# Kernel tuning notes

Measured on AMD Instinct MI355X. Metric: run time of the kernel, lower is better.

The kernel has to match this reference:

```python
import jax, jax.numpy as jnp
import numpy as np

EPS = 1e-5  # matches repo calc_mean_std eps


def _mvn(x):
    # mean-variance normalization per (B, C) over spatial dims, unbiased var (torch default)
    B, C, H, W = x.shape
    xf = x.reshape(B, C, H * W)
    m = xf.mean(-1, keepdims=True)
    v = xf.var(-1, ddof=1, keepdims=True)
    return ((xf - m) / jnp.sqrt(v + EPS)).reshape(x.shape)


def _conv1x1(x, w, b):
    # 1x1 conv == per-pixel channel mixing
    return jnp.einsum('oc,bchw->bohw', w, x) + b[None, :, None, None]


def _content_sa(x, Wp, bp):
    B, C, H, W = x.shape
    n = H * W
    xn = _mvn(x)
    q = _conv1x1(xn, Wp[0], bp[0]).reshape(B, C, n)  # f
    k = _conv1x1(xn, Wp[1], bp[1]).reshape(B, C, n)  # g
    energy = jnp.einsum('bci,bcj->bij', q, k)        # [B, N, N]
    attn = jax.nn.softmax(energy, axis=-1)
    v = _conv1x1(x, Wp[2], bp[2]).reshape(B, C, n)   # h
    out = jnp.einsum('bcj,bij->bci', v, attn).reshape(B, C, H, W)
    return _conv1x1(out, Wp[3], bp[3]) + x


def _style_sa(x, Wp, bp):
    B, C, H, W = x.shape
    n = H * W
    f = _conv1x1(x, Wp[0], bp[0]).reshape(B, C, n)
    g = _conv1x1(x, Wp[1], bp[1]).reshape(B, C, n)
    energy = jnp.einsum('bci,bdi->bcd', f, g)        # [B, C, C] channel attention
    attn = jax.nn.softmax(energy, axis=-1)
    h = _conv1x1(_mvn(x), Wp[2], bp[2]).reshape(B, C, n)
    out = jnp.einsum('bdc,bdi->bci', attn, h).reshape(B, C, H, W)  # attn^T @ h
    return _conv1x1(out, Wp[3], bp[3]) + x


def _ca(c, s, Wp, bp):
    B, C, Hc, Wc = c.shape
    nc = Hc * Wc
    _, _, Hs, Ws = s.shape
    ns = Hs * Ws
    q = _conv1x1(_mvn(c), Wp[0], bp[0]).reshape(B, C, nc)
    k = _conv1x1(_mvn(s), Wp[1], bp[1]).reshape(B, C, ns)
    energy = jnp.einsum('bci,bcj->bij', q, k)        # [B, Nc, Ns]
    attn = jax.nn.softmax(energy, axis=-1)
    v = _conv1x1(s, Wp[2], bp[2]).reshape(B, C, ns)
    out = jnp.einsum('bcj,bij->bci', v, attn).reshape(B, C, Hc, Wc)
    return _conv1x1(out, Wp[3], bp[3]) + c


def setup_inputs() -> dict:
    key = jax.random.key(0)
    ks = jax.random.split(key, 8)
    B, C, H, W = 4, 512, 64, 64
    scale = 0.02
    return {
        'content_feat': jax.random.normal(ks[0], (B, C, H, W), jnp.float32),
        'style_feat': jax.random.normal(ks[1], (B, C, H, W), jnp.float32),
        'csa_w': jax.random.normal(ks[2], (4, C, C), jnp.float32) * scale,
        'csa_b': jnp.zeros((4, C), jnp.float32),
        'ssa_w': jax.random.normal(ks[3], (4, C, C), jnp.float32) * scale,
        'ssa_b': jnp.zeros((4, C), jnp.float32),
        'ca_w': jax.random.normal(ks[4], (4, C, C), jnp.float32) * scale,
        'ca_b': jnp.zeros((4, C), jnp.float32),
    }


def reference(content_feat, style_feat, csa_w, csa_b, ssa_w, ssa_b, ca_w, ca_b):
    cf = _content_sa(content_feat, csa_w, csa_b)
    sf = _style_sa(style_feat, ssa_w, ssa_b)
    return _ca(cf, sf, ca_w, ca_b)
```

## Files before the change

kernel.cpp:

```cpp
#include <hip/hip_runtime.h>
#include <math.h>


#define B_ 4
#define C_ 512
#define N_ 4096
#define TM 128
#define TN 128

typedef unsigned short u16;
typedef __attribute__((ext_vector_type(8))) short s8v;
typedef __attribute__((ext_vector_type(4))) float f4v;

__device__ __forceinline__ u16 f2bf(float x) {
  unsigned u = __float_as_uint(x);
  return (u16)((u + 0x7fffu + ((u >> 16) & 1u)) >> 16);
}

__device__ __forceinline__ void gload16(const void* g, void* l) {
  __builtin_amdgcn_global_load_lds(
      (const __attribute__((address_space(1))) unsigned int*)g,
      (__attribute__((address_space(3))) unsigned int*)l, 16, 0, 0);
}

__device__ __forceinline__ float wave_red_sum(float v) {
#pragma unroll
  for (int off = 32; off > 0; off >>= 1) v += __shfl_xor(v, off, 64);
  return v;
}
__device__ __forceinline__ float wave_red_max(float v) {
#pragma unroll
  for (int off = 32; off > 0; off >>= 1) v = fmaxf(v, __shfl_xor(v, off, 64));
  return v;
}

__global__ __launch_bounds__(256) void row_stats_k(const float* __restrict__ x,
                                                   float* __restrict__ mean,
                                                   float* __restrict__ rstd) {
  long row = blockIdx.x;
  const float* p = x + row * (long)N_;
  int t = threadIdx.x;
  float s = 0.f, ss = 0.f;
  for (int i = t * 4; i < N_; i += 1024) {
    float4 v = *(const float4*)(p + i);
    s += v.x + v.y + v.z + v.w;
    ss += v.x * v.x + v.y * v.y + v.z * v.z + v.w * v.w;
  }
  __shared__ float rs_[4], rss_[4];
  int wid = t >> 6, lane = t & 63;
  s = wave_red_sum(s);
  ss = wave_red_sum(ss);
  if (lane == 0) { rs_[wid] = s; rss_[wid] = ss; }
  __syncthreads();
  if (t == 0) {
    float S = rs_[0] + rs_[1] + rs_[2] + rs_[3];
    float SS = rss_[0] + rss_[1] + rss_[2] + rss_[3];
    float m = S / (float)N_;
    float var = (SS - (float)N_ * m * m) / (float)(N_ - 1);
    mean[row] = m;
    rstd[row] = rsqrtf(var + 1e-5f);
  }
}

__global__ __launch_bounds__(256) void cvt_arr_k(const float* __restrict__ in,
                                                 u16* __restrict__ o, long n) {
  long i = ((long)blockIdx.x * 256 + threadIdx.x) * 4;
  if (i >= n) return;
  float4 v = *(const float4*)(in + i);
  *(ushort4*)(o + i) =
      make_ushort4(f2bf(v.x), f2bf(v.y), f2bf(v.z), f2bf(v.w));
}

template <bool HAS2>
__global__ __launch_bounds__(256) void t_cvt_k(
    const float* __restrict__ X, const float* __restrict__ mean,
    const float* __restrict__ rstd, u16* __restrict__ o1,
    u16* __restrict__ o2) {
  __shared__ float tile[64][68];
  const int b = blockIdx.z;
  const int c0 = blockIdx.y * 64, i0 = blockIdx.x * 64;
  const int t = threadIdx.x;
  const int tr = t >> 4, tc = (t & 15) << 2;
  const long CN = (long)C_ * N_;
  const float* Xb = X + (long)b * CN;
#pragma unroll
  for (int p2 = 0; p2 < 4; ++p2) {
    int c = p2 * 16 + tr;
    float4 v = *(const float4*)(Xb + (long)(c0 + c) * N_ + i0 + tc);
    tile[c][tc] = v.x;
    tile[c][tc + 1] = v.y;
    tile[c][tc + 2] = v.z;
    tile[c][tc + 3] = v.w;
  }
  __syncthreads();
  float mv[4], rv[4];
#pragma unroll
  for (int j = 0; j < 4; ++j) {
    mv[j] = mean[b * C_ + c0 + tc + j];
    rv[j] = rstd[b * C_ + c0 + tc + j];
  }
#pragma unroll
  for (int p2 = 0; p2 < 4; ++p2) {
    int ir = p2 * 16 + tr;
    long off = (long)b * CN + (long)(i0 + ir) * C_ + c0 + tc;
    u16 h1[4], h2[4];
#pragma unroll
    for (int j = 0; j < 4; ++j) {
      float v = tile[tc + j][ir];
      if (HAS2) h2[j] = f2bf(v);
      h1[j] = f2bf((v - mv[j]) * rv[j]);
    }
    *(ushort4*)(o1 + off) = make_ushort4(h1[0], h1[1], h1[2], h1[3]);
    if (HAS2) *(ushort4*)(o2 + off) = make_ushort4(h2[0], h2[1], h2[2], h2[3]);
  }
}

__global__ __launch_bounds__(256) void softmax_bf_k(const float* __restrict__ E,
                                                    u16* __restrict__ ph) {
  long row = blockIdx.x;
  const float* p = E + row * (long)N_;
  int t = threadIdx.x;
  float v[16];
  float mx = -3.4e38f;
#pragma unroll
  for (int q = 0; q < 4; ++q) {
    float4 w4 = *(const float4*)(p + t * 16 + q * 4);
    v[q * 4 + 0] = w4.x;
    v[q * 4 + 1] = w4.y;
    v[q * 4 + 2] = w4.z;
    v[q * 4 + 3] = w4.w;
    mx = fmaxf(mx, fmaxf(fmaxf(w4.x, w4.y), fmaxf(w4.z, w4.w)));
  }
  __shared__ float red[4];
  int wid = t >> 6, lane = t & 63;
  mx = wave_red_max(mx);
  if (lane == 0) red[wid] = mx;
  __syncthreads();
  mx = fmaxf(fmaxf(red[0], red[1]), fmaxf(red[2], red[3]));
  float s = 0.f;
#pragma unroll
  for (int i = 0; i < 16; ++i) {
    v[i] = __expf(v[i] - mx);
    s += v[i];
  }
  __syncthreads();
  s = wave_red_sum(s);
  if (lane == 0) red[wid] = s;
  __syncthreads();
  s = red[0] + red[1] + red[2] + red[3];
  float inv = 1.f / s;
  long ob = row * (long)N_ + t * 16;
#pragma unroll
  for (int q = 0; q < 4; ++q) {
    *(ushort4*)(ph + ob + q * 4) =
        make_ushort4(f2bf(v[q * 4 + 0] * inv), f2bf(v[q * 4 + 1] * inv),
                     f2bf(v[q * 4 + 2] * inv), f2bf(v[q * 4 + 3] * inv));
  }
}

__global__ __launch_bounds__(256) void softmax_t_k(const float* __restrict__ E2,
                                                   u16* __restrict__ ph) {
  int b = blockIdx.x >> 9;
  int x = blockIdx.x & 511;
  const float* p = E2 + ((long)b * C_ + x) * C_;
  int t = threadIdx.x;
  float v0 = p[t * 2], v1 = p[t * 2 + 1];
  float mx = fmaxf(v0, v1);
  __shared__ float red[4];
  int wid = t >> 6, lane = t & 63;
  mx = wave_red_max(mx);
  if (lane == 0) red[wid] = mx;
  __syncthreads();
  mx = fmaxf(fmaxf(red[0], red[1]), fmaxf(red[2], red[3]));
  v0 = __expf(v0 - mx);
  v1 = __expf(v1 - mx);
  float s = v0 + v1;
  __syncthreads();
  s = wave_red_sum(s);
  if (lane == 0) red[wid] = s;
  __syncthreads();
  s = red[0] + red[1] + red[2] + red[3];
  float inv = 1.f / s;
  long base = (long)b * C_ * C_;
  ph[base + (long)(t * 2) * C_ + x] = f2bf(v0 * inv);
  ph[base + (long)(t * 2 + 1) * C_ + x] = f2bf(v1 * inv);
}

template <bool BFOUT>
__global__ __launch_bounds__(256) void redk_k(
    const float* __restrict__ P, long pKS, long perB, int nsplit,
    float* __restrict__ of, u16* __restrict__ oh, long oBS, long oOff,
    long total) {
  long e = ((long)blockIdx.x * 256 + threadIdx.x) * 4;
  if (e >= total) return;
  long b = e / perB, rem = e - b * perB;
  const float* p0 = P + b * perB + rem;
  float4 s = *(const float4*)p0;
  for (int k = 1; k < nsplit; ++k) {
    float4 t = *(const float4*)(p0 + (long)k * pKS);
    s.x += t.x;
    s.y += t.y;
    s.z += t.z;
    s.w += t.w;
  }
  if (BFOUT) {
    *(ushort4*)(oh + b * oBS + oOff + rem) =
        make_ushort4(f2bf(s.x), f2bf(s.y), f2bf(s.z), f2bf(s.w));
  } else {
    *(float4*)(of + b * perB + rem) = s;
  }
}

template <int OUTM, int BIAS, bool RES>
__global__ __launch_bounds__(256, 3) void mm_k(
    const u16* __restrict__ Ap, long aBS, int lda,
    const u16* __restrict__ Bp, long bBS, int ldb,
    float* Of, u16* __restrict__ Obf, long oBS, long oKS, int ldo,
    const float* __restrict__ bias, const float* resp, long rBS,
    int K, int nsplit) {
  __shared__ u16 lds[16384];
  const int b = blockIdx.z / nsplit;
  const int ks = blockIdx.z % nsplit;
  const int Kc = K / nsplit;
  const int k0beg = ks * Kc;
  const int m0 = blockIdx.y * TM, n0 = blockIdx.x * TN;
  const int t = threadIdx.x, lane = t & 63, wid = t >> 6;
  const int wm = (wid >> 1) * 64, wn = (wid & 1) * 64;

  const u16* srcp = (wid < 2) ? (Ap + (long)b * aBS) : (Bp + (long)b * bBS);
  const int sld = (wid < 2) ? lda : ldb;
  const long srow0 = ((wid < 2) ? m0 : n0) + (wid & 1) * 64;
  u16* dstb = &lds[wid * 4096];
  const int srg = lane >> 3;
  const int ssl = lane & 7;

  f4v acc[4][4];
#pragma unroll
  for (int i = 0; i < 4; ++i)
#pragma unroll
    for (int j = 0; j < 4; ++j) acc[i][j] = (f4v){0.f, 0.f, 0.f, 0.f};

  const int lr = lane & 15, ksl = lane >> 4;
  const u16* lA = &lds[0];
  const u16* lB = &lds[8192];

  for (int k0 = k0beg; k0 < k0beg + Kc; k0 += 64) {
#pragma unroll
    for (int s = 0; s < 8; ++s) {
      int r = s * 8 + srg;
      int kb = ((ssl ^ (r & 7)) << 4);
      const u16* gp = srcp + (srow0 + r) * (long)sld + k0;
      gload16((const char*)gp + kb, dstb + s * 512);
    }
    __syncthreads();
#pragma unroll
    for (int kk = 0; kk < 2; ++kk) {
      s8v ar[4], br[4];
#pragma unroll
      for (int f = 0; f < 4; ++f) {
        int ra = wm + f * 16 + lr;
        ar[f] = *(const s8v*)(lA + ra * 64 +
                              ((((kk << 2) | ksl) ^ (ra & 7)) << 3));
        int rb = wn + f * 16 + lr;
        br[f] = *(const s8v*)(lB + rb * 64 +
                              ((((kk << 2) | ksl) ^ (rb & 7)) << 3));
      }
#pragma unroll
      for (int i = 0; i < 4; ++i)
#pragma unroll
        for (int j = 0; j < 4; ++j)
          acc[i][j] = __builtin_amdgcn_mfma_f32_16x16x32_bf16(
              ar[i], br[j], acc[i][j], 0, 0, 0);
    }
    __syncthreads();
  }

  const float* resb = RES ? (resp + (long)b * rBS) : nullptr;
  long obase = (long)b * oBS + (long)ks * oKS;
#pragma unroll
  for (int i = 0; i < 4; ++i) {
#pragma unroll
    for (int j = 0; j < 4; ++j) {
#pragma unroll
      for (int e = 0; e < 4; ++e) {
        int m = m0 + wm + i * 16 + ksl * 4 + e;
        int n = n0 + wn + j * 16 + lr;
        float v = acc[i][j][e];
        if (BIAS == 1) v += bias[m];
        if (BIAS == 2) v += bias[n];
        long o = obase + (long)m * ldo + n;
        if (OUTM == 0) {
          if (RES) v += resb[(long)m * ldo + n];
          Of[o] = v;
        } else {
          Obf[o] = f2bf(v);
        }
      }
    }
  }
}

extern "C" void kernel_launch(void* const* d_in, const int* in_sizes, int n_in,
                              void* d_out, int out_size, void* d_ws,
                              size_t ws_size, hipStream_t stream) {
  (void)in_sizes; (void)n_in; (void)out_size;
  const long CN = (long)C_ * N_;
  const long CC = (long)C_ * C_;

  const float* xc = (const float*)d_in[0];
  const float* xs = (const float*)d_in[1];
  const float* cw = (const float*)d_in[2];
  const float* cb = (const float*)d_in[3];
  const float* sw = (const float*)d_in[4];
  const float* sb = (const float*)d_in[5];
  const float* aw = (const float*)d_in[6];
  const float* ab = (const float*)d_in[7];
  float* out = (float*)d_out;

  char* w = (char*)d_ws;
  auto carve = [&](size_t bytes) {
    char* r = w;
    w += (bytes + 255) & ~(size_t)255;
    return r;
  };
  u16* cwb = (u16*)carve(4 * CC * 2);
  u16* swb = (u16*)carve(4 * CC * 2);
  u16* awb = (u16*)carve(4 * CC * 2);
  float* stats = (float*)carve(8 * B_ * C_ * 4);
  float* m1 = stats, *r1 = m1 + B_ * C_, *m2 = r1 + B_ * C_, *r2 = m2 + B_ * C_;
  float* m3 = r2 + B_ * C_, *r3 = m3 + B_ * C_, *m4 = r3 + B_ * C_,
       *r4 = m4 + B_ * C_;
  float* E2buf = (float*)carve(B_ * CC * 4);
  u16* aT = (u16*)carve(B_ * CC * 2);
  const size_t SLOT = (size_t)B_ * CN * 4;
  char* s0 = carve(SLOT);
  char* s1 = carve(SLOT);
  char* s2 = carve(SLOT);
  char* s3 = carve(SLOT);
  size_t used = (size_t)(w - (char*)d_ws);
  int S = N_;
  while (S > 128 && used + (size_t)6 * B_ * S * N_ > ws_size) S >>= 1;
  float* Ereg = (float*)carve((size_t)B_ * S * N_ * 4);
  u16* atB = (u16*)carve((size_t)B_ * S * N_ * 2);

  u16* sA = (u16*)s0;
  u16* sB = (u16*)s1;
  u16* sC = (u16*)s2;
  u16* sD = (u16*)s3;

  const int nsPV = N_ / S;
  const int e2s = 8;

  dim3 blk(256);
  dim3 gQ(4, 32, B_);
  dim3 gV(32, 4, B_);
  dim3 gTs(N_ / 64, C_ / 64, B_);

  cvt_arr_k<<<1024, blk, 0, stream>>>(cw, cwb, 4 * CC);
  cvt_arr_k<<<1024, blk, 0, stream>>>(sw, swb, 4 * CC);
  cvt_arr_k<<<1024, blk, 0, stream>>>(aw, awb, 4 * CC);

  auto attention = [&](const u16* Qn, const u16* Kn, const u16* Vp,
                       u16* oT) {
    for (int i0 = 0; i0 < N_; i0 += S) {
      mm_k<0, 0, false><<<dim3(N_ / TN, S / TM, B_), blk, 0, stream>>>(
          Qn + (long)i0 * C_, CN, C_, Kn, CN, C_, Ereg, nullptr,
          (long)S * N_, 0, N_, nullptr, nullptr, 0, C_, 1);
      softmax_bf_k<<<B_ * S, blk, 0, stream>>>(Ereg, atB);
      if (nsPV == 1) {
        mm_k<1, 0, false><<<dim3(C_ / TN, S / TM, B_), blk, 0, stream>>>(
            atB, (long)S * N_, N_, Vp, CN, N_, nullptr, oT + (long)i0 * C_,
            CN, 0, C_, nullptr, nullptr, 0, N_, 1);
      } else {
        mm_k<0, 0, false><<<dim3(C_ / TN, S / TM, B_ * nsPV), blk, 0,
                            stream>>>(
            atB, (long)S * N_, N_, Vp, CN, N_, Ereg, nullptr, (long)S * C_,
            (long)B_ * S * C_, C_, nullptr, nullptr, 0, N_, nsPV);
        redk_k<true><<<(B_ * S * C_) / 1024, blk, 0, stream>>>(
            Ereg, (long)B_ * S * C_, (long)S * C_, nsPV, nullptr, oT, CN,
            (long)i0 * C_, (long)B_ * S * C_);
      }
    }
  };

  row_stats_k<<<B_ * C_, blk, 0, stream>>>(xc, m1, r1);
  t_cvt_k<true><<<gTs, blk, 0, stream>>>(xc, m1, r1, sA, sB);
  mm_k<1, 2, false><<<gQ, blk, 0, stream>>>(sA, CN, C_, cwb, 0, C_, nullptr,
      sC, CN, 0, C_, cb, nullptr, 0, C_, 1);
  mm_k<1, 2, false><<<gQ, blk, 0, stream>>>(sA, CN, C_, cwb + CC, 0, C_,
      nullptr, sD, CN, 0, C_, cb + C_, nullptr, 0, C_, 1);
  mm_k<1, 1, false><<<gV, blk, 0, stream>>>(cwb + 2 * CC, 0, C_, sB, CN, C_,
      nullptr, sA, CN, 0, N_, cb + 2 * C_, nullptr, 0, C_, 1);
  attention(sC, sD, sA, sB);
  mm_k<0, 1, true><<<gV, blk, 0, stream>>>(cwb + 3 * CC, 0, C_, sB, CN, C_,
      out, nullptr, CN, 0, N_, cb + 3 * C_, xc, CN, C_, 1);

  row_stats_k<<<B_ * C_, blk, 0, stream>>>(xs, m2, r2);
  t_cvt_k<true><<<gTs, blk, 0, stream>>>(xs, m2, r2, sA, sC);
  mm_k<1, 1, false><<<gV, blk, 0, stream>>>(swb, 0, C_, sC, CN, C_, nullptr,
      sB, CN, 0, N_, sb, nullptr, 0, C_, 1);
  mm_k<1, 1, false><<<gV, blk, 0, stream>>>(swb + CC, 0, C_, sC, CN, C_,
      nullptr, sD, CN, 0, N_, sb + C_, nullptr, 0, C_, 1);
  mm_k<1, 2, false><<<gQ, blk, 0, stream>>>(sA, CN, C_, swb + 2 * CC, 0, C_,
      nullptr, sC, CN, 0, C_, sb + 2 * C_, nullptr, 0, C_, 1);
  mm_k<0, 0, false><<<dim3(4, 4, B_ * e2s), blk, 0, stream>>>(
      sB, CN, N_, sD, CN, N_, Ereg, nullptr, CC, (long)B_ * CC, C_, nullptr,
      nullptr, 0, N_, e2s);
  redk_k<false><<<(B_ * (int)CC) / 1024, blk, 0, stream>>>(
      Ereg, (long)B_ * CC, CC, e2s, E2buf, nullptr, 0, 0, (long)B_ * CC);
  softmax_t_k<<<B_ * C_, blk, 0, stream>>>(E2buf, aT);
  mm_k<1, 0, false><<<gQ, blk, 0, stream>>>(sC, CN, C_, aT, CC, C_, nullptr,
      sA, CN, 0, C_, nullptr, nullptr, 0, C_, 1);
  float* sfF = (float*)s1;
  mm_k<0, 1, true><<<gV, blk, 0, stream>>>(swb + 3 * CC, 0, C_, sA, CN, C_,
      sfF, nullptr, CN, 0, N_, sb + 3 * C_, xs, CN, C_, 1);

  row_stats_k<<<B_ * C_, blk, 0, stream>>>(out, m3, r3);
  row_stats_k<<<B_ * C_, blk, 0, stream>>>(sfF, m4, r4);
  t_cvt_k<false><<<gTs, blk, 0, stream>>>(out, m3, r3, sC, nullptr);
  t_cvt_k<true><<<gTs, blk, 0, stream>>>(sfF, m4, r4, sD, sA);
  mm_k<1, 2, false><<<gQ, blk, 0, stream>>>(sC, CN, C_, awb, 0, C_, nullptr,
      sB, CN, 0, C_, ab, nullptr, 0, C_, 1);
  mm_k<1, 2, false><<<gQ, blk, 0, stream>>>(sD, CN, C_, awb + CC, 0, C_,
      nullptr, sC, CN, 0, C_, ab + C_, nullptr, 0, C_, 1);
  mm_k<1, 1, false><<<gV, blk, 0, stream>>>(awb + 2 * CC, 0, C_, sA, CN, C_,
      nullptr, sD, CN, 0, N_, ab + 2 * C_, nullptr, 0, C_, 1);
  attention(sB, sC, sD, sA);
  mm_k<0, 1, true><<<gV, blk, 0, stream>>>(awb + 3 * CC, 0, C_, sA, CN, C_,
      out, nullptr, CN, 0, N_, ab + 3 * C_, out, CN, C_, 1);
}
```

Before: 1.008 ms.

## Store attention energies in fp16, fuse Q/K projections, merge weight conversions

Attention energy matrices are now written as fp16 instead of fp32, which halves the energy round-trip traffic and lets the workspace hold larger row chunks, so the split-K PV path and its reduction kernel are dropped. The content Q/K projections and the style f/g projections are each fused into a single GEMM writing an interleaved 1024-wide output. The three weight-conversion launches become one kernel, and the style row-stats launch is hoisted earlier. The trade-off is reduced energy precision (fp16 range and rounding) ahead of softmax, and a hard requirement that the workspace fits the larger chunk, since the split path is gone.

```diff
diff --git a/kernel.cpp b/kernel.cpp
--- a/kernel.cpp
+++ b/kernel.cpp
@@ -15,6 +15,16 @@
 __device__ __forceinline__ u16 f2bf(float x) {
   unsigned u = __float_as_uint(x);
   return (u16)((u + 0x7fffu + ((u >> 16) & 1u)) >> 16);
+}
+__device__ __forceinline__ u16 f2h(float x) {
+  union { _Float16 h; u16 u; } z;
+  z.h = (_Float16)x;
+  return z.u;
+}
+__device__ __forceinline__ float h2f(u16 v) {
+  union { _Float16 h; u16 u; } z;
+  z.u = v;
+  return (float)z.h;
 }
 
 __device__ __forceinline__ void gload16(const void* g, void* l) {
@@ -62,13 +72,16 @@
   }
 }
 
-__global__ __launch_bounds__(256) void cvt_arr_k(const float* __restrict__ in,
-                                                 u16* __restrict__ o, long n) {
+__global__ __launch_bounds__(256) void cvt3_k(
+    const float* __restrict__ a, const float* __restrict__ b,
+    const float* __restrict__ c, u16* __restrict__ oa, u16* __restrict__ ob,
+    u16* __restrict__ oc, long n) {
+  const float* in = blockIdx.y == 0 ? a : (blockIdx.y == 1 ? b : c);
+  u16* o = blockIdx.y == 0 ? oa : (blockIdx.y == 1 ? ob : oc);
   long i = ((long)blockIdx.x * 256 + threadIdx.x) * 4;
   if (i >= n) return;
   float4 v = *(const float4*)(in + i);
-  *(ushort4*)(o + i) =
-      make_ushort4(f2bf(v.x), f2bf(v.y), f2bf(v.z), f2bf(v.w));
+  *(ushort4*)(o + i) = make_ushort4(f2bf(v.x), f2bf(v.y), f2bf(v.z), f2bf(v.w));
 }
 
 template <bool HAS2>
@@ -115,21 +128,22 @@
   }
 }
 
-__global__ __launch_bounds__(256) void softmax_bf_k(const float* __restrict__ E,
+__global__ __launch_bounds__(256) void softmax_bf_k(const u16* __restrict__ E,
                                                     u16* __restrict__ ph) {
   long row = blockIdx.x;
-  const float* p = E + row * (long)N_;
+  const u16* p = E + row * (long)N_;
   int t = threadIdx.x;
   float v[16];
   float mx = -3.4e38f;
 #pragma unroll
   for (int q = 0; q < 4; ++q) {
-    float4 w4 = *(const float4*)(p + t * 16 + q * 4);
-    v[q * 4 + 0] = w4.x;
-    v[q * 4 + 1] = w4.y;
-    v[q * 4 + 2] = w4.z;
-    v[q * 4 + 3] = w4.w;
-    mx = fmaxf(mx, fmaxf(fmaxf(w4.x, w4.y), fmaxf(w4.z, w4.w)));
+    ushort4 w4 = *(const ushort4*)(p + t * 16 + q * 4);
+    v[q * 4 + 0] = h2f(w4.x);
+    v[q * 4 + 1] = h2f(w4.y);
+    v[q * 4 + 2] = h2f(w4.z);
+    v[q * 4 + 3] = h2f(w4.w);
+    mx = fmaxf(mx, fmaxf(fmaxf(v[q * 4], v[q * 4 + 1]),
+                         fmaxf(v[q * 4 + 2], v[q * 4 + 3])));
   }
   __shared__ float red[4];
   int wid = t >> 6, lane = t & 63;
@@ -186,11 +200,10 @@
   ph[base + (long)(t * 2 + 1) * C_ + x] = f2bf(v1 * inv);
 }
 
-template <bool BFOUT>
-__global__ __launch_bounds__(256) void redk_k(
-    const float* __restrict__ P, long pKS, long perB, int nsplit,
-    float* __restrict__ of, u16* __restrict__ oh, long oBS, long oOff,
-    long total) {
+__global__ __launch_bounds__(256) void redk_k(const float* __restrict__ P,
+                                              long pKS, long perB, int nsplit,
+                                              float* __restrict__ of,
+                                              long total) {
   long e = ((long)blockIdx.x * 256 + threadIdx.x) * 4;
   if (e >= total) return;
   long b = e / perB, rem = e - b * perB;
@@ -203,12 +216,7 @@
     s.z += t.z;
     s.w += t.w;
   }
-  if (BFOUT) {
-    *(ushort4*)(oh + b * oBS + oOff + rem) =
-        make_ushort4(f2bf(s.x), f2bf(s.y), f2bf(s.z), f2bf(s.w));
-  } else {
-    *(float4*)(of + b * perB + rem) = s;
-  }
+  *(float4*)(of + b * perB + rem) = s;
 }
 
 template <int OUTM, int BIAS, bool RES>
@@ -292,8 +300,10 @@
         if (OUTM == 0) {
           if (RES) v += resb[(long)m * ldo + n];
           Of[o] = v;
+        } else if (OUTM == 1) {
+          Obf[o] = f2bf(v);
         } else {
-          Obf[o] = f2bf(v);
+          Obf[o] = f2h(v);
         }
       }
     }
@@ -339,77 +349,64 @@
   char* s3 = carve(SLOT);
   size_t used = (size_t)(w - (char*)d_ws);
   int S = N_;
-  while (S > 128 && used + (size_t)6 * B_ * S * N_ > ws_size) S >>= 1;
-  float* Ereg = (float*)carve((size_t)B_ * S * N_ * 4);
+  while (S > 128 && used + (size_t)4 * B_ * S * N_ > ws_size) S >>= 1;
+  u16* Ereg16 = (u16*)carve((size_t)B_ * S * N_ * 2);
   u16* atB = (u16*)carve((size_t)B_ * S * N_ * 2);
+  float* EregF = (float*)Ereg16;
 
   u16* sA = (u16*)s0;
   u16* sB = (u16*)s1;
   u16* sC = (u16*)s2;
   u16* sD = (u16*)s3;
 
-  const int nsPV = N_ / S;
   const int e2s = 8;
 
   dim3 blk(256);
   dim3 gQ(4, 32, B_);
   dim3 gV(32, 4, B_);
+  dim3 gQK(8, 32, B_);
+  dim3 gFG(32, 8, B_);
   dim3 gTs(N_ / 64, C_ / 64, B_);
 
-  cvt_arr_k<<<1024, blk, 0, stream>>>(cw, cwb, 4 * CC);
-  cvt_arr_k<<<1024, blk, 0, stream>>>(sw, swb, 4 * CC);
-  cvt_arr_k<<<1024, blk, 0, stream>>>(aw, awb, 4 * CC);
-
-  auto attention = [&](const u16* Qn, const u16* Kn, const u16* Vp,
-                       u16* oT) {
+  cvt3_k<<<dim3(1024, 3), blk, 0, stream>>>(cw, sw, aw, cwb, swb, awb, 4 * CC);
+
+  auto attention = [&](const u16* Qp, int ldq, long qBS, const u16* Kp,
+                       int ldk, long kBS, const u16* Vp, u16* oT) {
     for (int i0 = 0; i0 < N_; i0 += S) {
-      mm_k<0, 0, false><<<dim3(N_ / TN, S / TM, B_), blk, 0, stream>>>(
-          Qn + (long)i0 * C_, CN, C_, Kn, CN, C_, Ereg, nullptr,
+      mm_k<2, 0, false><<<dim3(N_ / TN, S / TM, B_), blk, 0, stream>>>(
+          Qp + (long)i0 * ldq, qBS, ldq, Kp, kBS, ldk, nullptr, Ereg16,
           (long)S * N_, 0, N_, nullptr, nullptr, 0, C_, 1);
-      softmax_bf_k<<<B_ * S, blk, 0, stream>>>(Ereg, atB);
-      if (nsPV == 1) {
-        mm_k<1, 0, false><<<dim3(C_ / TN, S / TM, B_), blk, 0, stream>>>(
-            atB, (long)S * N_, N_, Vp, CN, N_, nullptr, oT + (long)i0 * C_,
-            CN, 0, C_, nullptr, nullptr, 0, N_, 1);
-      } else {
-        mm_k<0, 0, false><<<dim3(C_ / TN, S / TM, B_ * nsPV), blk, 0,
-                            stream>>>(
-            atB, (long)S * N_, N_, Vp, CN, N_, Ereg, nullptr, (long)S * C_,
-            (long)B_ * S * C_, C_, nullptr, nullptr, 0, N_, nsPV);
-        redk_k<true><<<(B_ * S * C_) / 1024, blk, 0, stream>>>(
-            Ereg, (long)B_ * S * C_, (long)S * C_, nsPV, nullptr, oT, CN,
-            (long)i0 * C_, (long)B_ * S * C_);
-      }
+      softmax_bf_k<<<B_ * S, blk, 0, stream>>>(Ereg16, atB);
+      mm_k<1, 0, false><<<dim3(C_ / TN, S / TM, B_), blk, 0, stream>>>(
+          atB, (long)S * N_, N_, Vp, CN, N_, nullptr, oT + (long)i0 * C_, CN,
+          0, C_, nullptr, nullptr, 0, N_, 1);
     }
   };
 
   row_stats_k<<<B_ * C_, blk, 0, stream>>>(xc, m1, r1);
+  row_stats_k<<<B_ * C_, blk, 0, stream>>>(xs, m2, r2);
   t_cvt_k<true><<<gTs, blk, 0, stream>>>(xc, m1, r1, sA, sB);
-  mm_k<1, 2, false><<<gQ, blk, 0, stream>>>(sA, CN, C_, cwb, 0, C_, nullptr,
-      sC, CN, 0, C_, cb, nullptr, 0, C_, 1);
-  mm_k<1, 2, false><<<gQ, blk, 0, stream>>>(sA, CN, C_, cwb + CC, 0, C_,
-      nullptr, sD, CN, 0, C_, cb + C_, nullptr, 0, C_, 1);
+  mm_k<1, 2, false><<<gQK, blk, 0, stream>>>(sA, CN, C_, cwb, 0, C_, nullptr,
+      sC, (long)N_ * 1024, 0, 1024, cb, nullptr, 0, C_, 1);
   mm_k<1, 1, false><<<gV, blk, 0, stream>>>(cwb + 2 * CC, 0, C_, sB, CN, C_,
-      nullptr, sA, CN, 0, N_, cb + 2 * C_, nullptr, 0, C_, 1);
-  attention(sC, sD, sA, sB);
-  mm_k<0, 1, true><<<gV, blk, 0, stream>>>(cwb + 3 * CC, 0, C_, sB, CN, C_,
+      nullptr, sD, CN, 0, N_, cb + 2 * C_, nullptr, 0, C_, 1);
+  attention(sC, 1024, (long)N_ * 1024, sC + 512, 1024, (long)N_ * 1024, sD,
+            sA);
+  mm_k<0, 1, true><<<gV, blk, 0, stream>>>(cwb + 3 * CC, 0, C_, sA, CN, C_,
       out, nullptr, CN, 0, N_, cb + 3 * C_, xc, CN, C_, 1);
 
-  row_stats_k<<<B_ * C_, blk, 0, stream>>>(xs, m2, r2);
   t_cvt_k<true><<<gTs, blk, 0, stream>>>(xs, m2, r2, sA, sC);
-  mm_k<1, 1, false><<<gV, blk, 0, stream>>>(swb, 0, C_, sC, CN, C_, nullptr,
-      sB, CN, 0, N_, sb, nullptr, 0, C_, 1);
-  mm_k<1, 1, false><<<gV, blk, 0, stream>>>(swb + CC, 0, C_, sC, CN, C_,
-      nullptr, sD, CN, 0, N_, sb + C_, nullptr, 0, C_, 1);
+  mm_k<1, 1, false><<<gFG, blk, 0, stream>>>(swb, 0, C_, sC, CN, C_, nullptr,
+      sD, (long)1024 * N_, 0, N_, sb, nullptr, 0, C_, 1);
   mm_k<1, 2, false><<<gQ, blk, 0, stream>>>(sA, CN, C_, swb + 2 * CC, 0, C_,
-      nullptr, sC, CN, 0, C_, sb + 2 * C_, nullptr, 0, C_, 1);
+      nullptr, sB, CN, 0, C_, sb + 2 * C_, nullptr, 0, C_, 1);
   mm_k<0, 0, false><<<dim3(4, 4, B_ * e2s), blk, 0, stream>>>(
-      sB, CN, N_, sD, CN, N_, Ereg, nullptr, CC, (long)B_ * CC, C_, nullptr,
-      nullptr, 0, N_, e2s);
-  redk_k<false><<<(B_ * (int)CC) / 1024, blk, 0, stream>>>(
-      Ereg, (long)B_ * CC, CC, e2s, E2buf, nullptr, 0, 0, (long)B_ * CC);
+      sD, (long)1024 * N_, N_, sD + (long)512 * N_, (long)1024 * N_, N_,
+      EregF, nullptr, CC, (long)B_ * CC, C_, nullptr, nullptr, 0, N_, e2s);
+  redk_k<<<(B_ * (int)CC) / 1024, blk, 0, stream>>>(
+      EregF, (long)B_ * CC, CC, e2s, E2buf, (long)B_ * CC);
   softmax_t_k<<<B_ * C_, blk, 0, stream>>>(E2buf, aT);
-  mm_k<1, 0, false><<<gQ, blk, 0, stream>>>(sC, CN, C_, aT, CC, C_, nullptr,
+  mm_k<1, 0, false><<<gQ, blk, 0, stream>>>(sB, CN, C_, aT, CC, C_, nullptr,
       sA, CN, 0, C_, nullptr, nullptr, 0, C_, 1);
   float* sfF = (float*)s1;
   mm_k<0, 1, true><<<gV, blk, 0, stream>>>(swb + 3 * CC, 0, C_, sA, CN, C_,
@@ -425,7 +422,7 @@
       nullptr, sC, CN, 0, C_, ab + C_, nullptr, 0, C_, 1);
   mm_k<1, 1, false><<<gV, blk, 0, stream>>>(awb + 2 * CC, 0, C_, sA, CN, C_,
       nullptr, sD, CN, 0, N_, ab + 2 * C_, nullptr, 0, C_, 1);
-  attention(sB, sC, sD, sA);
+  attention(sB, C_, CN, sC, C_, CN, sD, sA);
   mm_k<0, 1, true><<<gV, blk, 0, stream>>>(awb + 3 * CC, 0, C_, sA, CN, C_,
       out, nullptr, CN, 0, N_, ab + 3 * C_, out, CN, C_, 1);
 }
```

Measured after the change: 1.139 ms. +13.0%, slower.
